# Optimization experiments

Hardware: AMD Instinct MI355X
Metric: run time of the kernel (lower is better)

Reference implementation:

```python
import jax, jax.numpy as jnp
import numpy as np

N_LAYERS = 4
D = 768
H = 12
DK = D // H
FF = 2048
SD = 5
DIM_LOC = 6
EPS = 1e-10


def layer_norm(x, g, b, eps=1e-5):
    m = x.mean(-1, keepdims=True)
    v = ((x - m) ** 2).mean(-1, keepdims=True)
    return (x - m) / jnp.sqrt(v + eps) * g + b


def calc_pairwise_locs(centers):
    # centers: [b, l, 3] -> [b, l, t, 5] spatial relation features ('center' type, dist-normalized)
    rel = centers[:, :, None, :] - centers[:, None, :, :]
    d = jnp.sqrt(jnp.sum(rel ** 2, -1) + EPS)
    max_d = jnp.max(d.reshape(d.shape[0], -1), -1)
    dn = d / max_d[:, None, None]
    d2 = jnp.sqrt(jnp.sum(rel[..., :2] ** 2, -1) + EPS)
    return jnp.stack([dn, rel[..., 2] / d, d2 / d, rel[..., 1] / d2, rel[..., 0] / d2], -1)


def setup_inputs() -> dict:
    key = jax.random.key(0)
    ks = jax.random.split(key, 32)
    B, L = 16, 512
    std = 0.02
    inp = {
        'obj_embeds': jax.random.normal(ks[0], (B, L, D), jnp.float32),
        'obj_locs': jax.random.uniform(ks[1], (B, L, DIM_LOC), jnp.float32) * 5.0,
        'obj_masks': jnp.ones((B, L), jnp.bool_),
        # single loc layer (obj_loc_encoding='same_all')
        'loc_w': jax.random.normal(ks[2], (DIM_LOC, D), jnp.float32) * std,
        'loc_b': jnp.zeros((D,), jnp.float32),
        'loc_ln_g': jnp.ones((D,), jnp.float32),
        'loc_ln_b': jnp.zeros((D,), jnp.float32),
        # per-layer params, stacked on leading layer dim
        'Wq': jax.random.normal(ks[3], (N_LAYERS, D, D), jnp.float32) * std,
        'bq': jnp.zeros((N_LAYERS, D), jnp.float32),
        'Wk': jax.random.normal(ks[4], (N_LAYERS, D, D), jnp.float32) * std,
        'bk': jnp.zeros((N_LAYERS, D), jnp.float32),
        'Wv': jax.random.normal(ks[5], (N_LAYERS, D, D), jnp.float32) * std,
        'bv': jnp.zeros((N_LAYERS, D), jnp.float32),
        'Wfc': jax.random.normal(ks[6], (N_LAYERS, D, D), jnp.float32) * std,
        'bfc': jnp.zeros((N_LAYERS, D), jnp.float32),
        'loc_fc_w': jax.random.normal(ks[7], (N_LAYERS, SD, H), jnp.float32) * std,
        'loc_fc_b': jnp.zeros((N_LAYERS, H), jnp.float32),
        'ln0_g': jnp.ones((N_LAYERS, D), jnp.float32),
        'ln0_b': jnp.zeros((N_LAYERS, D), jnp.float32),
        'W1': jax.random.normal(ks[8], (N_LAYERS, D, FF), jnp.float32) * std,
        'b1': jnp.zeros((N_LAYERS, FF), jnp.float32),
        'W2': jax.random.normal(ks[9], (N_LAYERS, FF, D), jnp.float32) * std,
        'b2': jnp.zeros((N_LAYERS, D), jnp.float32),
        'ln1_g': jnp.ones((N_LAYERS, D), jnp.float32),
        'ln1_b': jnp.zeros((N_LAYERS, D), jnp.float32),
        'ln2_g': jnp.ones((N_LAYERS, D), jnp.float32),
        'ln2_b': jnp.zeros((N_LAYERS, D), jnp.float32),
    }
    return inp


def _forward(obj_embeds, obj_locs, obj_masks, loc_w, loc_b, loc_ln_g, loc_ln_b,
             Wq, bq, Wk, bk, Wv, bv, Wfc, bfc, loc_fc_w, loc_fc_b, ln0_g, ln0_b,
             W1, b1, W2, b2, ln1_g, ln1_b, ln2_g, ln2_b):
    B, L, _ = obj_embeds.shape
    pl = calc_pairwise_locs(obj_locs[..., :3])        # [b,l,t,5]
    kpm = jnp.logical_not(obj_masks)                  # key_padding_mask: True = pad
    mask = kpm[:, None, None, :]                      # [b,1,1,t]
    query_pos = layer_norm(obj_locs @ loc_w + loc_b, loc_ln_g, loc_ln_b)
    x = obj_embeds
    scale = np.float32(1.0 / np.sqrt(DK))
    for i in range(N_LAYERS):
        x = x + query_pos  # obj_loc_encoding='same_all': add loc embedding every layer
        res = x
        q = (x @ Wq[i] + bq[i]).reshape(B, L, H, DK)
        k = (x @ Wk[i] + bk[i]).reshape(B, L, H, DK)
        v = (x @ Wv[i] + bv[i]).reshape(B, L, H, DK)
        attn = jnp.einsum('blhk,bthk->bhlt', q, k) * scale
        loc_attn = jax.nn.relu(jnp.einsum('bltd,dh->bhlt', pl, loc_fc_w[i])
                               + loc_fc_b[i][None, :, None, None])
        attn = jnp.where(mask, -1e30, attn)
        loc_attn = jnp.where(mask, 0.0, loc_attn)
        fused = jax.nn.softmax(jnp.log(jnp.clip(loc_attn, 1e-6)) + attn, axis=-1)
        out = jnp.einsum('bhlt,bthv->blhv', fused, v).reshape(B, L, D)
        out = out @ Wfc[i] + bfc[i]
        x2 = layer_norm(out + res, ln0_g[i], ln0_b[i])   # attn-internal residual + LN
        x = layer_norm(x + x2, ln1_g[i], ln1_b[i])       # encoder-layer norm1
        ff = jax.nn.gelu(x @ W1[i] + b1[i], approximate=False) @ W2[i] + b2[i]
        x = layer_norm(x + ff, ln2_g[i], ln2_b[i])       # encoder-layer norm2
    return x


def reference(obj_embeds, obj_locs, obj_masks, loc_w, loc_b, loc_ln_g, loc_ln_b,
              Wq, bq, Wk, bk, Wv, bv, Wfc, bfc, loc_fc_w, loc_fc_b, ln0_g, ln0_b,
              W1, b1, W2, b2, ln1_g, ln1_b, ln2_g, ln2_b):
    return _forward(obj_embeds, obj_locs, obj_masks, loc_w, loc_b, loc_ln_g, loc_ln_b,
                    Wq, bq, Wk, bk, Wv, bv, Wfc, bfc, loc_fc_w, loc_fc_b, ln0_g, ln0_b,
                    W1, b1, W2, b2, ln1_g, ln1_b, ln2_g, ln2_b)
```

## Files before the change

### kernel.cpp

```cpp
#include <hip/hip_runtime.h>
#include <hip/hip_bf16.h>
#include <math.h>

#define NL 4
#define D 768
#define H 12
#define DK 64
#define FF 2048
#define SD 5
#define DLOC 6
#define B 16
#define L 512
#define M (B*L)

typedef unsigned short u16;
typedef unsigned int u32;
typedef __attribute__((ext_vector_type(8))) __bf16 bf16x8;
typedef __attribute__((ext_vector_type(4))) float f32x4;

__device__ inline float b2f(u16 u){ u32 v = ((u32)u)<<16; return __builtin_bit_cast(float, v); }
__device__ inline u16 f2b(float f){ __hip_bfloat16 h = __float2bfloat16(f); return __builtin_bit_cast(u16, h); }

__device__ inline void gld16(const u16* g, u16* l) {
    __builtin_amdgcn_global_load_lds(
        (const __attribute__((address_space(1))) u32*)(const void*)g,
        (__attribute__((address_space(3))) u32*)(void*)l, 16, 0, 0);
}

__global__ __launch_bounds__(256) void maxd_kernel(const float* __restrict__ locs,
                                                   u32* __restrict__ maxd) {
    int b = blockIdx.x >> 5;
    int seg = blockIdx.x & 31;
    __shared__ float cx[L], cy[L], cz[L];
    for (int i = threadIdx.x; i < L; i += 256) {
        const float* p = locs + ((size_t)b*L + i)*DLOC;
        cx[i] = p[0]; cy[i] = p[1]; cz[i] = p[2];
    }
    __syncthreads();
    float mx = 0.f;
    int r0 = seg*16;
    #pragma unroll
    for (int r = 0; r < 16; ++r) {
        float px = cx[r0+r], py = cy[r0+r], pz = cz[r0+r];
        for (int c = threadIdx.x; c < L; c += 256) {
            float dx = px-cx[c], dy = py-cy[c], dz = pz-cz[c];
            mx = fmaxf(mx, dx*dx + dy*dy + dz*dz);
        }
    }
    #pragma unroll
    for (int m=1;m<64;m<<=1) mx = fmaxf(mx, __shfl_xor(mx, m));
    __shared__ float wred[4];
    if ((threadIdx.x & 63) == 0) wred[threadIdx.x >> 6] = mx;
    __syncthreads();
    if (threadIdx.x == 0) {
        float v = fmaxf(fmaxf(wred[0],wred[1]), fmaxf(wred[2],wred[3]));
        float d = sqrtf(v + 1e-10f);
        atomicMax(maxd + b, __builtin_bit_cast(u32, d));
    }
}

__global__ __launch_bounds__(256) void initq_kernel(const float* __restrict__ embeds,
    const float* __restrict__ locs, const float* __restrict__ lw, const float* __restrict__ lb,
    const float* __restrict__ lg, const float* __restrict__ lbb,
    float* __restrict__ x, u16* __restrict__ xb) {
    int row = blockIdx.x;
    float lc[DLOC];
    #pragma unroll
    for (int d=0; d<DLOC; d++) lc[d] = locs[(size_t)row*DLOC + d];
    float mv[3], s1 = 0.f, s2 = 0.f;
    #pragma unroll
    for (int e = 0; e < 3; e++) {
        int col = threadIdx.x + 256*e;
        float v = lb[col];
        #pragma unroll
        for (int d = 0; d < DLOC; d++) v += lc[d]*lw[d*D + col];
        mv[e] = v; s1 += v; s2 += v*v;
    }
    __shared__ float r1[256], r2[256];
    r1[threadIdx.x]=s1; r2[threadIdx.x]=s2; __syncthreads();
    for (int s=128;s>0;s>>=1){
        if(threadIdx.x<s){r1[threadIdx.x]+=r1[threadIdx.x+s]; r2[threadIdx.x]+=r2[threadIdx.x+s];}
        __syncthreads();
    }
    float mean = r1[0]*(1.0f/D);
    float var  = r2[0]*(1.0f/D) - mean*mean;
    float rstd = rsqrtf(var + 1e-5f);
    #pragma unroll
    for (int e=0;e<3;e++){
        int col = threadIdx.x+256*e;
        float qp = (mv[e]-mean)*rstd*lg[col]+lbb[col];
        float v = embeds[(size_t)row*D+col] + qp;
        x[(size_t)row*D+col] = v;
        xb[(size_t)row*D+col] = f2b(v);
    }
}

__global__ __launch_bounds__(256) void ln01_kernel(const float* __restrict__ t0f,
    const float* __restrict__ xin,
    const float* __restrict__ g0, const float* __restrict__ b0,
    const float* __restrict__ g1, const float* __restrict__ b1,
    float* __restrict__ xout, u16* __restrict__ xb) {
    int row = blockIdx.x;
    __shared__ float r1[256], r2[256];
    float xv[3], vv[3], s1=0.f, s2=0.f;
    #pragma unroll
    for (int e=0;e<3;e++){
        int col = threadIdx.x+256*e;
        float xr = xin[(size_t)row*D+col];
        float v = t0f[(size_t)row*D+col] + xr;
        xv[e]=xr; vv[e]=v; s1+=v; s2+=v*v;
    }
    r1[threadIdx.x]=s1; r2[threadIdx.x]=s2; __syncthreads();
    for (int s=128;s>0;s>>=1){
        if(threadIdx.x<s){r1[threadIdx.x]+=r1[threadIdx.x+s]; r2[threadIdx.x]+=r2[threadIdx.x+s];}
        __syncthreads();
    }
    float mean0 = r1[0]*(1.0f/D);
    float var0  = r2[0]*(1.0f/D) - mean0*mean0;
    float rstd0 = rsqrtf(var0 + 1e-5f);
    __syncthreads();
    float uv[3]; s1=0.f; s2=0.f;
    #pragma unroll
    for (int e=0;e<3;e++){
        int col = threadIdx.x+256*e;
        float x2 = (vv[e]-mean0)*rstd0*g0[col]+b0[col];
        float u = xv[e] + x2;
        uv[e]=u; s1+=u; s2+=u*u;
    }
    r1[threadIdx.x]=s1; r2[threadIdx.x]=s2; __syncthreads();
    for (int s=128;s>0;s>>=1){
        if(threadIdx.x<s){r1[threadIdx.x]+=r1[threadIdx.x+s]; r2[threadIdx.x]+=r2[threadIdx.x+s];}
        __syncthreads();
    }
    float mean1 = r1[0]*(1.0f/D);
    float var1  = r2[0]*(1.0f/D) - mean1*mean1;
    float rstd1 = rsqrtf(var1 + 1e-5f);
    #pragma unroll
    for (int e=0;e<3;e++){
        int col = threadIdx.x+256*e;
        float v = (uv[e]-mean1)*rstd1*g1[col]+b1[col];
        xout[(size_t)row*D+col] = v;
        xb[(size_t)row*D+col] = f2b(v);
    }
}

template<int LAST>
__global__ __launch_bounds__(256) void ln2q_kernel(const float* __restrict__ xin,
    const float* __restrict__ t0f, const float* __restrict__ g2, const float* __restrict__ b2,
    const float* __restrict__ locs, const float* __restrict__ lw, const float* __restrict__ lb,
    const float* __restrict__ lg, const float* __restrict__ lbb,
    float* __restrict__ xout, u16* __restrict__ xb) {
    int row = blockIdx.x;
    __shared__ float r1[256], r2[256], r3[256], r4[256];
    float lc[DLOC];
    if (!LAST) {
        #pragma unroll
        for (int d=0; d<DLOC; d++) lc[d] = locs[(size_t)row*DLOC + d];
    }
    float vv[3], mv[3], s1=0.f, s2=0.f, s3=0.f, s4=0.f;
    #pragma unroll
    for (int e=0;e<3;e++){
        int col = threadIdx.x+256*e;
        float v = xin[(size_t)row*D+col] + t0f[(size_t)row*D+col];
        vv[e]=v; s1+=v; s2+=v*v;
        if (!LAST) {
            float mvv = lb[col];
            #pragma unroll
            for (int d = 0; d < DLOC; d++) mvv += lc[d]*lw[d*D + col];
            mv[e]=mvv; s3+=mvv; s4+=mvv*mvv;
        }
    }
    r1[threadIdx.x]=s1; r2[threadIdx.x]=s2;
    if (!LAST) { r3[threadIdx.x]=s3; r4[threadIdx.x]=s4; }
    __syncthreads();
    for (int s=128;s>0;s>>=1){
        if(threadIdx.x<s){
            r1[threadIdx.x]+=r1[threadIdx.x+s]; r2[threadIdx.x]+=r2[threadIdx.x+s];
            if (!LAST){ r3[threadIdx.x]+=r3[threadIdx.x+s]; r4[threadIdx.x]+=r4[threadIdx.x+s]; }
        }
        __syncthreads();
    }
    float mean = r1[0]*(1.0f/D);
    float var  = r2[0]*(1.0f/D) - mean*mean;
    float rstd = rsqrtf(var + 1e-5f);
    float mean3=0.f, rstd3=0.f;
    if (!LAST) {
        mean3 = r3[0]*(1.0f/D);
        float var3 = r4[0]*(1.0f/D) - mean3*mean3;
        rstd3 = rsqrtf(var3 + 1e-5f);
    }
    #pragma unroll
    for (int e=0;e<3;e++){
        int col = threadIdx.x+256*e;
        float xn = (vv[e]-mean)*rstd*g2[col]+b2[col];
        if (LAST) {
            xout[(size_t)row*D+col] = xn;
        } else {
            float qp = (mv[e]-mean3)*rstd3*lg[col]+lbb[col];
            float v = xn + qp;
            xout[(size_t)row*D+col] = v;
            xb[(size_t)row*D+col] = f2b(v);
        }
    }
}

__global__ __launch_bounds__(256) void convT6_kernel(
    const float* __restrict__ Wq, const float* __restrict__ Wk,
    const float* __restrict__ Wv, const float* __restrict__ Wfc,
    const float* __restrict__ W1, const float* __restrict__ W2,
    u16* __restrict__ wq_t, u16* __restrict__ wfc_t,
    u16* __restrict__ w1_t, u16* __restrict__ w2_t) {
    int bid = blockIdx.x;
    const float* in; u16* outp; int K, N, nb, kb;
    if (bid < 1728) {
        int m = bid / 576, r = bid % 576;
        in = (m==0) ? Wq : (m==1) ? Wk : Wv;
        outp = wq_t + m*D*D; K = D; N = D; nb = r % 24; kb = r / 24;
    } else if (bid < 2304) {
        int r = bid - 1728;
        in = Wfc; outp = wfc_t; K = D; N = D; nb = r % 24; kb = r / 24;
    } else if (bid < 3840) {
        int r = bid - 2304;
        in = W1; outp = w1_t; K = D; N = FF; nb = r % 64; kb = r / 64;
    } else {
        int r = bid - 3840;
        in = W2; outp = w2_t; K = FF; N = D; nb = r % 24; kb = r / 24;
    }
    __shared__ float tile[32][33];
    int kbb = kb*32, nbb = nb*32;
    int tx = threadIdx.x & 31, ty = threadIdx.x >> 5;
    #pragma unroll
    for (int i=0;i<32;i+=8)
        tile[ty+i][tx] = in[(size_t)(kbb+ty+i)*N + nbb+tx];
    __syncthreads();
    #pragma unroll
    for (int i=0;i<32;i+=8)
        outp[(size_t)(nbb+ty+i)*K + kbb+tx] = f2b(tile[tx][ty+i]);
}

__global__ __launch_bounds__(256) void biaspack_kernel(const float* __restrict__ bq,
    const float* __restrict__ bk, const float* __restrict__ bv, float* __restrict__ outb) {
    int i = blockIdx.x*256 + threadIdx.x;
    int l = i / (3*D), j = i % (3*D);
    float v = (j < D) ? bq[l*D + j] : (j < 2*D ? bk[l*D + j - D] : bv[l*D + j - 2*D]);
    outb[i] = v;
}

template<int OUT_BF16, int ACT>
__global__ __launch_bounds__(256) void mm_kernel(
    const u16* __restrict__ A, const u16* __restrict__ Bt,
    const float* __restrict__ bias, void* __restrict__ Cout, int K, int N)
{
    __shared__ u16 As[2][128*32];
    __shared__ u16 Bs[2][128*32];
    const int tid = threadIdx.x;
    const int lane = tid & 63, wv = tid >> 6;
    const int m0 = blockIdx.y*128, n0 = blockIdx.x*128;
    const int wm = (wv>>1)*64, wn = (wv&1)*64;

    const u16* ag = A  + (size_t)(m0 + wv*16 + (lane>>2))*K + (lane&3)*8;
    const u16* bg = Bt + (size_t)(n0 + wv*16 + (lane>>2))*K + (lane&3)*8;
    const size_t rstep = (size_t)64*K;
    const int lofs = wv*512;

    f32x4 acc[4][4];
    #pragma unroll
    for (int i=0;i<4;i++)
        #pragma unroll
        for (int j=0;j<4;j++) acc[i][j] = (f32x4){0.f,0.f,0.f,0.f};

    const int lr = lane & 15, kq = lane >> 4;

    gld16(ag, &As[0][lofs]);
    gld16(ag + rstep, &As[0][2048+lofs]);
    gld16(bg, &Bs[0][lofs]);
    gld16(bg + rstep, &Bs[0][2048+lofs]);
    __syncthreads();

    int cur = 0;
    for (int k0 = 0; k0 < K; k0 += 32) {
        if (k0 + 32 < K) {
            int nx = cur ^ 1, kn = k0 + 32;
            gld16(ag + kn, &As[nx][lofs]);
            gld16(ag + rstep + kn, &As[nx][2048+lofs]);
            gld16(bg + kn, &Bs[nx][lofs]);
            gld16(bg + rstep + kn, &Bs[nx][2048+lofs]);
        }
        const u16* Arow = &As[cur][(wm + lr)*32 + kq*8];
        const u16* Brow = &Bs[cur][(wn + lr)*32 + kq*8];
        bf16x8 af[4], bfr[4];
        #pragma unroll
        for (int i=0;i<4;i++) af[i]  = *(const bf16x8*)(Arow + i*512);
        #pragma unroll
        for (int j=0;j<4;j++) bfr[j] = *(const bf16x8*)(Brow + j*512);
        #pragma unroll
        for (int i=0;i<4;i++)
            #pragma unroll
            for (int j=0;j<4;j++)
                acc[i][j] = __builtin_amdgcn_mfma_f32_16x16x32_bf16(af[i], bfr[j], acc[i][j], 0,0,0);
        __syncthreads();
        cur ^= 1;
    }

    const int cr = (lane>>4)*4, cc = lane & 15;
    #pragma unroll
    for (int i=0;i<4;i++) {
        int row = m0 + wm + i*16 + cr;
        #pragma unroll
        for (int j=0;j<4;j++) {
            int col = n0 + wn + j*16 + cc;
            float bv_ = bias[col];
            #pragma unroll
            for (int r=0;r<4;r++) {
                float v = acc[i][j][r] + bv_;
                if (ACT) v = 0.5f*v*(1.0f + erff(v*0.70710678f));
                if (OUT_BF16) ((u16*)Cout)[(size_t)(row+r)*N + col] = f2b(v);
                else        ((float*)Cout)[(size_t)(row+r)*N + col] = v;
            }
        }
    }
}

__global__ __launch_bounds__(256) void attn_kernel(
    const u16* __restrict__ qkv, const float* __restrict__ locs,
    const float* __restrict__ maxdp, const float* __restrict__ lfw,
    const float* __restrict__ lfb, u16* __restrict__ out)
{
    const int RS = 3*D;
    const float SC = 0.18033688f;
    const int bid = blockIdx.x;
    const int qt = bid & 7;
    const int hp = (bid >> 3) % 6;
    const int b  = bid / 48;
    const int qb = qt*64;
    const int h0 = hp*2;

    __shared__ u16 Ks[2][64*64];
    __shared__ u16 Vt[2][64*64];
    __shared__ u16 Pl[2][4*16*64];
    __shared__ float Cts[64][4];

    const int t = threadIdx.x;
    const int lane = t & 63, wv = t >> 6;
    const int l15 = lane & 15, l4 = lane >> 4;

    bf16x8 qf[2][2];
    {
        const u16* qr = qkv + (size_t)(b*L + qb + wv*16 + l15)*RS + h0*DK + l4*8;
        qf[0][0] = *(const bf16x8*)(qr);
        qf[0][1] = *(const bf16x8*)(qr + 32);
        qf[1][0] = *(const bf16x8*)(qr + DK);
        qf[1][1] = *(const bf16x8*)(qr + DK + 32);
    }
    float cqx[4], cqy[4], cqz[4];
    #pragma unroll
    for (int r=0;r<4;r++){
        const float* p = locs + (size_t)(b*L + qb + wv*16 + l4*4 + r)*DLOC;
        cqx[r]=p[0]; cqy[r]=p[1]; cqz[r]=p[2];
    }
    const float invmd = 1.0f / maxdp[b];
    float w0p[2], w1[2], w2[2], w3[2], w4[2], wbb[2];
    #pragma unroll
    for (int hh=0; hh<2; hh++){
        int h = h0+hh;
        w0p[hh] = lfw[0*H+h]*invmd; w1[hh]=lfw[1*H+h]; w2[hh]=lfw[2*H+h];
        w3[hh]=lfw[3*H+h]; w4[hh]=lfw[4*H+h]; wbb[hh]=lfb[h];
    }

    f32x4 oacc[2][4];
    float mrun[2][4], lrun[2][4];
    #pragma unroll
    for (int hh=0;hh<2;hh++)
        #pragma unroll
        for (int j=0;j<4;j++){ oacc[hh][j] = (f32x4){0.f,0.f,0.f,0.f};
                               mrun[hh][j] = -1e30f; lrun[hh][j] = 0.f; }

    const int srow0 = (wv*64 + lane) >> 3;
    const int sslot = lane & 7;

    for (int kt = 0; kt < L; kt += 64) {
        const u16* kgb = qkv + (size_t)(b*L + kt)*RS + D + h0*DK;
        {
            int r0 = srow0, r1 = srow0 + 32;
            int c0 = (sslot ^ (r0&7))*8, c1 = (sslot ^ (r1&7))*8;
            gld16(kgb + (size_t)r0*RS + c0, &Ks[0][wv*512]);
            gld16(kgb + (size_t)r1*RS + c1, &Ks[0][2048 + wv*512]);
            gld16(kgb + DK + (size_t)r0*RS + c0, &Ks[1][wv*512]);
            gld16(kgb + DK + (size_t)r1*RS + c1, &Ks[1][2048 + wv*512]);
        }
        #pragma unroll
        for (int hh=0; hh<2; hh++){
            const u16* vp = qkv + (size_t)(b*L + kt + lane)*RS + 2*D + (h0+hh)*DK + wv*16;
            bf16x8 v0 = *(const bf16x8*)(vp);
            bf16x8 v1 = *(const bf16x8*)(vp + 8);
            int d0 = wv*16;
            #pragma unroll
            for (int e=0;e<8;e++){
                Vt[hh][(d0+e)*64   + (lane ^ (e<<3))] = ((const u16*)&v0)[e];
                Vt[hh][(d0+8+e)*64 + (lane ^ (e<<3))] = ((const u16*)&v1)[e];
            }
        }
        if (t < 64) {
            #pragma unroll
            for (int d=0;d<3;d++) Cts[t][d] = locs[(size_t)(b*L + kt + t)*DLOC + d];
        }
        __syncthreads();

        f32x4 sacc[2][4];
        #pragma unroll
        for (int hh=0;hh<2;hh++)
            #pragma unroll
            for (int j=0;j<4;j++){
                sacc[hh][j] = (f32x4){0.f,0.f,0.f,0.f};
                #pragma unroll
                for (int c=0;c<2;c++){
                    int row = j*16 + l15;
                    int slot = l4 + 4*c;
                    bf16x8 kf = *(const bf16x8*)(&Ks[hh][row*64 + ((slot ^ (row&7))*8)]);
                    sacc[hh][j] = __builtin_amdgcn_mfma_f32_16x16x32_bf16(qf[hh][c], kf, sacc[hh][j], 0,0,0);
                }
            }

        float ctx[4], cty[4], ctz[4];
        #pragma unroll
        for (int j=0;j<4;j++){
            int c = l15 + 16*j;
            ctx[j]=Cts[c][0]; cty[j]=Cts[c][1]; ctz[j]=Cts[c][2];
        }

        float alr[2][4];
        #pragma unroll
        for (int r=0;r<4;r++){
            float f0[4], f1[4], f2[4], f3[4], f4[4];
            #pragma unroll
            for (int j=0;j<4;j++){
                float rx = cqx[r]-ctx[j], ry = cqy[r]-cty[j], rz = cqz[r]-ctz[j];
                float d2e = fmaf(ry,ry, fmaf(rx,rx, 1e-10f));
                float r2  = fmaf(rz,rz, d2e);
                float invd  = __builtin_amdgcn_rsqf(r2);
                float invd2 = __builtin_amdgcn_rsqf(d2e);
                f0[j] = r2*invd;
                f1[j] = rz*invd;
                f2[j] = (d2e*invd2)*invd;
                f3[j] = ry*invd2;
                f4[j] = rx*invd2;
            }
            #pragma unroll
            for (int hh=0; hh<2; hh++){
                float sv[4], la[4];
                #pragma unroll
                for (int j=0;j<4;j++){
                    float z = fmaf(f0[j], w0p[hh],
                              fmaf(f1[j], w1[hh],
                              fmaf(f2[j], w2[hh],
                              fmaf(f3[j], w3[hh],
                              fmaf(f4[j], w4[hh], wbb[hh])))));
                    la[j] = fmaxf(z, 1e-6f);
                    sv[j] = sacc[hh][j][r]*SC;
                }
                float mx = fmaxf(fmaxf(sv[0],sv[1]), fmaxf(sv[2],sv[3]));
                #pragma unroll
                for (int msk=1; msk<16; msk<<=1) mx = fmaxf(mx, __shfl_xor(mx, msk));
                float mo = mrun[hh][r];
                float mn = fmaxf(mo, mx);
                float al = __builtin_amdgcn_exp2f(mo - mn);
                float sp = 0.f;
                u16* pw = &Pl[hh][wv*1024];
                int q = l4*4 + r, sw = (q&7)<<3;
                #pragma unroll
                for (int j=0;j<4;j++){
                    float p = la[j] * __builtin_amdgcn_exp2f(sv[j] - mn);
                    sp += p;
                    pw[q*64 + ((l15 + 16*j) ^ sw)] = f2b(p);
                }
                #pragma unroll
                for (int msk=1; msk<16; msk<<=1) sp += __shfl_xor(sp, msk);
                mrun[hh][r] = mn;
                lrun[hh][r] = lrun[hh][r]*al + sp;
                alr[hh][r] = al;
            }
        }

        #pragma unroll
        for (int hh=0; hh<2; hh++){
            #pragma unroll
            for (int j=0;j<4;j++)
                #pragma unroll
                for (int r=0;r<4;r++) oacc[hh][j][r] *= alr[hh][r];
            const u16* pr = &Pl[hh][wv*1024];
            #pragma unroll
            for (int c=0;c<2;c++){
                int prow = l15;
                int pslot = l4 + 4*c;
                bf16x8 pf = *(const bf16x8*)(pr + prow*64 + ((pslot ^ (prow&7))*8));
                #pragma unroll
                for (int j=0;j<4;j++){
                    int vrow = j*16 + l15;
                    int vslot = l4 + 4*c;
                    bf16x8 vf = *(const bf16x8*)(&Vt[hh][vrow*64 + ((vslot ^ (vrow&7))*8)]);
                    oacc[hh][j] = __builtin_amdgcn_mfma_f32_16x16x32_bf16(pf, vf, oacc[hh][j], 0,0,0);
                }
            }
        }
        __syncthreads();
    }

    #pragma unroll
    for (int hh=0; hh<2; hh++)
        #pragma unroll
        for (int r=0;r<4;r++){
            float inv = __builtin_amdgcn_rcpf(lrun[hh][r]);
            size_t obase = (size_t)(b*L + qb + wv*16 + l4*4 + r)*D + (h0+hh)*DK;
            #pragma unroll
            for (int j=0;j<4;j++)
                out[obase + l15 + 16*j] = f2b(oacc[hh][j][r] * inv);
        }
}

extern "C" void kernel_launch(void* const* d_in, const int* in_sizes, int n_in,
                              void* d_out, int out_size, void* d_ws, size_t ws_size,
                              hipStream_t stream) {
    const float* obj_embeds = (const float*)d_in[0];
    const float* obj_locs   = (const float*)d_in[1];
    const float* loc_w   = (const float*)d_in[3];
    const float* loc_b   = (const float*)d_in[4];
    const float* loc_ln_g= (const float*)d_in[5];
    const float* loc_ln_b= (const float*)d_in[6];
    const float* Wq = (const float*)d_in[7];
    const float* bq = (const float*)d_in[8];
    const float* Wk = (const float*)d_in[9];
    const float* bk = (const float*)d_in[10];
    const float* Wv = (const float*)d_in[11];
    const float* bv = (const float*)d_in[12];
    const float* Wfc= (const float*)d_in[13];
    const float* bfc= (const float*)d_in[14];
    const float* lfw= (const float*)d_in[15];
    const float* lfb= (const float*)d_in[16];
    const float* ln0_g = (const float*)d_in[17];
    const float* ln0_b = (const float*)d_in[18];
    const float* W1 = (const float*)d_in[19];
    const float* b1 = (const float*)d_in[20];
    const float* W2 = (const float*)d_in[21];
    const float* b2 = (const float*)d_in[22];
    const float* ln1_g = (const float*)d_in[23];
    const float* ln1_b = (const float*)d_in[24];
    const float* ln2_g = (const float*)d_in[25];
    const float* ln2_b = (const float*)d_in[26];

    float* x  = (float*)d_out;
    char* base = (char*)d_ws;
    u16*   xb    = (u16*)  (base);
    u16*   qkv   = (u16*)  (base + 12582912);
    u16*   aob   = (u16*)  (base + 50331648);
    float* t0f   = (float*)(base + 62914560);
    u16*   wq_t  = (u16*)  (base + 88080384);
    u16*   wfc_t = (u16*)  (base + 91619328);
    u16*   w1_t  = (u16*)  (base + 92798976);
    u16*   w2_t  = (u16*)  (base + 95944704);
    float* bqkv  = (float*)(base + 99090432);
    u32*   maxd  = (u32*)  (base + 99127296);
    u16*   h1b   = qkv;

    hipMemsetAsync(maxd, 0, B*sizeof(u32), stream);
    maxd_kernel<<<B*32, 256, 0, stream>>>(obj_locs, maxd);
    biaspack_kernel<<<(NL*3*D)/256, 256, 0, stream>>>(bq, bk, bv, bqkv);
    initq_kernel<<<M, 256, 0, stream>>>(obj_embeds, obj_locs, loc_w, loc_b,
                                        loc_ln_g, loc_ln_b, x, xb);

    for (int i = 0; i < NL; i++) {
        const size_t wo = (size_t)i*D*D;
        convT6_kernel<<<5376, 256, 0, stream>>>(Wq + wo, Wk + wo, Wv + wo, Wfc + wo,
                                                W1 + (size_t)i*D*FF, W2 + (size_t)i*FF*D,
                                                wq_t, wfc_t, w1_t, w2_t);

        mm_kernel<1,0><<<dim3(18,64), 256, 0, stream>>>(xb, wq_t, bqkv + i*3*D, qkv, D, 3*D);
        attn_kernel<<<B*6*8, 256, 0, stream>>>(qkv, obj_locs, (const float*)maxd,
                                               lfw + i*SD*H, lfb + i*H, aob);
        mm_kernel<0,0><<<dim3(6,64), 256, 0, stream>>>(aob, wfc_t, bfc + i*D, t0f, D, D);
        ln01_kernel<<<M, 256, 0, stream>>>(t0f, x, ln0_g + i*D, ln0_b + i*D,
                                           ln1_g + i*D, ln1_b + i*D, x, xb);
        mm_kernel<1,1><<<dim3(16,64), 256, 0, stream>>>(xb, w1_t, b1 + i*FF, h1b, D, FF);
        mm_kernel<0,0><<<dim3(6,64), 256, 0, stream>>>(h1b, w2_t, b2 + i*D, t0f, FF, D);
        if (i < NL-1)
            ln2q_kernel<0><<<M, 256, 0, stream>>>(x, t0f, ln2_g + i*D, ln2_b + i*D,
                obj_locs, loc_w, loc_b, loc_ln_g, loc_ln_b, x, xb);
        else
            ln2q_kernel<1><<<M, 256, 0, stream>>>(x, t0f, ln2_g + i*D, ln2_b + i*D,
                obj_locs, loc_w, loc_b, loc_ln_g, loc_ln_b, x, xb);
    }
}
```

Baseline: 1.214 ms.

## Vectorize layernorm kernels, widen weight transpose, remap GEMM tile order

The layernorm-style kernels (initq, ln01, ln2q) now use 192 threads, each handling four contiguous columns through float4 loads and stores. Their block reductions use wavefront shuffles and one small shared-memory step instead of a tree of __syncthreads. The weight transpose kernel uses float4 reads and ushort4 bf16 writes. The GEMM kernel remaps block IDs so consecutive blocks are spread across eight groups, likely to fit the MI355X's multiple-XCD layout and improve L2 locality. The aim is fewer memory transactions and less sync overhead in bandwidth-bound elementwise kernels, at the cost of extra remapping arithmetic and the assumption that grid sizes divide by 8.

```diff
diff --git a/kernel.cpp b/kernel.cpp
--- a/kernel.cpp
+++ b/kernel.cpp
@@ -59,148 +59,161 @@
     }
 }
 
-__global__ __launch_bounds__(256) void initq_kernel(const float* __restrict__ embeds,
+__global__ __launch_bounds__(192) void initq_kernel(const float* __restrict__ embeds,
     const float* __restrict__ locs, const float* __restrict__ lw, const float* __restrict__ lb,
     const float* __restrict__ lg, const float* __restrict__ lbb,
     float* __restrict__ x, u16* __restrict__ xb) {
     int row = blockIdx.x;
+    int c4 = threadIdx.x*4;
+    int lane = threadIdx.x & 63, wv = threadIdx.x >> 6;
     float lc[DLOC];
     #pragma unroll
     for (int d=0; d<DLOC; d++) lc[d] = locs[(size_t)row*DLOC + d];
-    float mv[3], s1 = 0.f, s2 = 0.f;
-    #pragma unroll
-    for (int e = 0; e < 3; e++) {
-        int col = threadIdx.x + 256*e;
-        float v = lb[col];
-        #pragma unroll
-        for (int d = 0; d < DLOC; d++) v += lc[d]*lw[d*D + col];
-        mv[e] = v; s1 += v; s2 += v*v;
-    }
-    __shared__ float r1[256], r2[256];
-    r1[threadIdx.x]=s1; r2[threadIdx.x]=s2; __syncthreads();
-    for (int s=128;s>0;s>>=1){
-        if(threadIdx.x<s){r1[threadIdx.x]+=r1[threadIdx.x+s]; r2[threadIdx.x]+=r2[threadIdx.x+s];}
-        __syncthreads();
-    }
-    float mean = r1[0]*(1.0f/D);
-    float var  = r2[0]*(1.0f/D) - mean*mean;
-    float rstd = rsqrtf(var + 1e-5f);
-    #pragma unroll
-    for (int e=0;e<3;e++){
-        int col = threadIdx.x+256*e;
-        float qp = (mv[e]-mean)*rstd*lg[col]+lbb[col];
-        float v = embeds[(size_t)row*D+col] + qp;
-        x[(size_t)row*D+col] = v;
-        xb[(size_t)row*D+col] = f2b(v);
-    }
-}
-
-__global__ __launch_bounds__(256) void ln01_kernel(const float* __restrict__ t0f,
+    float4 mv = *(const float4*)(lb + c4);
+    #pragma unroll
+    for (int d=0; d<DLOC; d++) {
+        float4 w = *(const float4*)(lw + d*D + c4);
+        mv.x = fmaf(lc[d], w.x, mv.x); mv.y = fmaf(lc[d], w.y, mv.y);
+        mv.z = fmaf(lc[d], w.z, mv.z); mv.w = fmaf(lc[d], w.w, mv.w);
+    }
+    float s1 = mv.x+mv.y+mv.z+mv.w;
+    float s2 = mv.x*mv.x+mv.y*mv.y+mv.z*mv.z+mv.w*mv.w;
+    #pragma unroll
+    for (int m=1;m<64;m<<=1){ s1 += __shfl_xor(s1,m); s2 += __shfl_xor(s2,m); }
+    __shared__ float a1[3], a2[3];
+    if (lane==0){ a1[wv]=s1; a2[wv]=s2; }
+    __syncthreads();
+    float S1 = a1[0]+a1[1]+a1[2], S2 = a2[0]+a2[1]+a2[2];
+    float mean = S1*(1.0f/D);
+    float rstd = rsqrtf(S2*(1.0f/D) - mean*mean + 1e-5f);
+    float4 G = *(const float4*)(lg + c4);
+    float4 Bb = *(const float4*)(lbb + c4);
+    float4 E = *(const float4*)(embeds + (size_t)row*D + c4);
+    float4 v;
+    v.x = E.x + (mv.x-mean)*rstd*G.x+Bb.x;
+    v.y = E.y + (mv.y-mean)*rstd*G.y+Bb.y;
+    v.z = E.z + (mv.z-mean)*rstd*G.z+Bb.z;
+    v.w = E.w + (mv.w-mean)*rstd*G.w+Bb.w;
+    *(float4*)(x + (size_t)row*D + c4) = v;
+    ushort4 u; u.x=f2b(v.x); u.y=f2b(v.y); u.z=f2b(v.z); u.w=f2b(v.w);
+    *(ushort4*)(xb + (size_t)row*D + c4) = u;
+}
+
+__global__ __launch_bounds__(192) void ln01_kernel(const float* __restrict__ t0f,
     const float* __restrict__ xin,
     const float* __restrict__ g0, const float* __restrict__ b0,
     const float* __restrict__ g1, const float* __restrict__ b1,
     float* __restrict__ xout, u16* __restrict__ xb) {
     int row = blockIdx.x;
-    __shared__ float r1[256], r2[256];
-    float xv[3], vv[3], s1=0.f, s2=0.f;
-    #pragma unroll
-    for (int e=0;e<3;e++){
-        int col = threadIdx.x+256*e;
-        float xr = xin[(size_t)row*D+col];
-        float v = t0f[(size_t)row*D+col] + xr;
-        xv[e]=xr; vv[e]=v; s1+=v; s2+=v*v;
-    }
-    r1[threadIdx.x]=s1; r2[threadIdx.x]=s2; __syncthreads();
-    for (int s=128;s>0;s>>=1){
-        if(threadIdx.x<s){r1[threadIdx.x]+=r1[threadIdx.x+s]; r2[threadIdx.x]+=r2[threadIdx.x+s];}
-        __syncthreads();
-    }
-    float mean0 = r1[0]*(1.0f/D);
-    float var0  = r2[0]*(1.0f/D) - mean0*mean0;
-    float rstd0 = rsqrtf(var0 + 1e-5f);
-    __syncthreads();
-    float uv[3]; s1=0.f; s2=0.f;
-    #pragma unroll
-    for (int e=0;e<3;e++){
-        int col = threadIdx.x+256*e;
-        float x2 = (vv[e]-mean0)*rstd0*g0[col]+b0[col];
-        float u = xv[e] + x2;
-        uv[e]=u; s1+=u; s2+=u*u;
-    }
-    r1[threadIdx.x]=s1; r2[threadIdx.x]=s2; __syncthreads();
-    for (int s=128;s>0;s>>=1){
-        if(threadIdx.x<s){r1[threadIdx.x]+=r1[threadIdx.x+s]; r2[threadIdx.x]+=r2[threadIdx.x+s];}
-        __syncthreads();
-    }
-    float mean1 = r1[0]*(1.0f/D);
-    float var1  = r2[0]*(1.0f/D) - mean1*mean1;
-    float rstd1 = rsqrtf(var1 + 1e-5f);
-    #pragma unroll
-    for (int e=0;e<3;e++){
-        int col = threadIdx.x+256*e;
-        float v = (uv[e]-mean1)*rstd1*g1[col]+b1[col];
-        xout[(size_t)row*D+col] = v;
-        xb[(size_t)row*D+col] = f2b(v);
-    }
+    int c4 = threadIdx.x*4;
+    int lane = threadIdx.x & 63, wv = threadIdx.x >> 6;
+    size_t base = (size_t)row*D + c4;
+    float4 xr = *(const float4*)(xin + base);
+    float4 tv = *(const float4*)(t0f + base);
+    float4 v = {xr.x+tv.x, xr.y+tv.y, xr.z+tv.z, xr.w+tv.w};
+    float s1 = v.x+v.y+v.z+v.w;
+    float s2 = v.x*v.x+v.y*v.y+v.z*v.z+v.w*v.w;
+    #pragma unroll
+    for (int m=1;m<64;m<<=1){ s1 += __shfl_xor(s1,m); s2 += __shfl_xor(s2,m); }
+    __shared__ float a1[3], a2[3], a3[3], a4[3];
+    if (lane==0){ a1[wv]=s1; a2[wv]=s2; }
+    __syncthreads();
+    float S1 = a1[0]+a1[1]+a1[2], S2 = a2[0]+a2[1]+a2[2];
+    float mean0 = S1*(1.0f/D);
+    float rstd0 = rsqrtf(S2*(1.0f/D) - mean0*mean0 + 1e-5f);
+    float4 G0 = *(const float4*)(g0 + c4);
+    float4 B0 = *(const float4*)(b0 + c4);
+    float4 u;
+    u.x = xr.x + (v.x-mean0)*rstd0*G0.x+B0.x;
+    u.y = xr.y + (v.y-mean0)*rstd0*G0.y+B0.y;
+    u.z = xr.z + (v.z-mean0)*rstd0*G0.z+B0.z;
+    u.w = xr.w + (v.w-mean0)*rstd0*G0.w+B0.w;
+    s1 = u.x+u.y+u.z+u.w;
+    s2 = u.x*u.x+u.y*u.y+u.z*u.z+u.w*u.w;
+    #pragma unroll
+    for (int m=1;m<64;m<<=1){ s1 += __shfl_xor(s1,m); s2 += __shfl_xor(s2,m); }
+    if (lane==0){ a3[wv]=s1; a4[wv]=s2; }
+    __syncthreads();
+    S1 = a3[0]+a3[1]+a3[2]; S2 = a4[0]+a4[1]+a4[2];
+    float mean1 = S1*(1.0f/D);
+    float rstd1 = rsqrtf(S2*(1.0f/D) - mean1*mean1 + 1e-5f);
+    float4 G1 = *(const float4*)(g1 + c4);
+    float4 B1 = *(const float4*)(b1 + c4);
+    float4 o;
+    o.x = (u.x-mean1)*rstd1*G1.x+B1.x;
+    o.y = (u.y-mean1)*rstd1*G1.y+B1.y;
+    o.z = (u.z-mean1)*rstd1*G1.z+B1.z;
+    o.w = (u.w-mean1)*rstd1*G1.w+B1.w;
+    *(float4*)(xout + base) = o;
+    ushort4 ub; ub.x=f2b(o.x); ub.y=f2b(o.y); ub.z=f2b(o.z); ub.w=f2b(o.w);
+    *(ushort4*)(xb + base) = ub;
 }
 
 template<int LAST>
-__global__ __launch_bounds__(256) void ln2q_kernel(const float* __restrict__ xin,
+__global__ __launch_bounds__(192) void ln2q_kernel(const float* __restrict__ xin,
     const float* __restrict__ t0f, const float* __restrict__ g2, const float* __restrict__ b2,
     const float* __restrict__ locs, const float* __restrict__ lw, const float* __restrict__ lb,
     const float* __restrict__ lg, const float* __restrict__ lbb,
     float* __restrict__ xout, u16* __restrict__ xb) {
     int row = blockIdx.x;
-    __shared__ float r1[256], r2[256], r3[256], r4[256];
-    float lc[DLOC];
+    int c4 = threadIdx.x*4;
+    int lane = threadIdx.x & 63, wv = threadIdx.x >> 6;
+    size_t base = (size_t)row*D + c4;
+    float4 xr = *(const float4*)(xin + base);
+    float4 tv = *(const float4*)(t0f + base);
+    float4 v = {xr.x+tv.x, xr.y+tv.y, xr.z+tv.z, xr.w+tv.w};
+    float s1 = v.x+v.y+v.z+v.w;
+    float s2 = v.x*v.x+v.y*v.y+v.z*v.z+v.w*v.w;
+    float s3 = 0.f, s4 = 0.f;
+    float4 mv = {0,0,0,0};
     if (!LAST) {
+        float lc[DLOC];
         #pragma unroll
         for (int d=0; d<DLOC; d++) lc[d] = locs[(size_t)row*DLOC + d];
-    }
-    float vv[3], mv[3], s1=0.f, s2=0.f, s3=0.f, s4=0.f;
-    #pragma unroll
-    for (int e=0;e<3;e++){
-        int col = threadIdx.x+256*e;
-        float v = xin[(size_t)row*D+col] + t0f[(size_t)row*D+col];
-        vv[e]=v; s1+=v; s2+=v*v;
-        if (!LAST) {
-            float mvv = lb[col];
-            #pragma unroll
-            for (int d = 0; d < DLOC; d++) mvv += lc[d]*lw[d*D + col];
-            mv[e]=mvv; s3+=mvv; s4+=mvv*mvv;
-        }
-    }
-    r1[threadIdx.x]=s1; r2[threadIdx.x]=s2;
-    if (!LAST) { r3[threadIdx.x]=s3; r4[threadIdx.x]=s4; }
-    __syncthreads();
-    for (int s=128;s>0;s>>=1){
-        if(threadIdx.x<s){
-            r1[threadIdx.x]+=r1[threadIdx.x+s]; r2[threadIdx.x]+=r2[threadIdx.x+s];
-            if (!LAST){ r3[threadIdx.x]+=r3[threadIdx.x+s]; r4[threadIdx.x]+=r4[threadIdx.x+s]; }
-        }
-        __syncthreads();
-    }
-    float mean = r1[0]*(1.0f/D);
-    float var  = r2[0]*(1.0f/D) - mean*mean;
-    float rstd = rsqrtf(var + 1e-5f);
-    float mean3=0.f, rstd3=0.f;
-    if (!LAST) {
-        mean3 = r3[0]*(1.0f/D);
-        float var3 = r4[0]*(1.0f/D) - mean3*mean3;
-        rstd3 = rsqrtf(var3 + 1e-5f);
-    }
-    #pragma unroll
-    for (int e=0;e<3;e++){
-        int col = threadIdx.x+256*e;
-        float xn = (vv[e]-mean)*rstd*g2[col]+b2[col];
-        if (LAST) {
-            xout[(size_t)row*D+col] = xn;
-        } else {
-            float qp = (mv[e]-mean3)*rstd3*lg[col]+lbb[col];
-            float v = xn + qp;
-            xout[(size_t)row*D+col] = v;
-            xb[(size_t)row*D+col] = f2b(v);
-        }
+        mv = *(const float4*)(lb + c4);
+        #pragma unroll
+        for (int d=0; d<DLOC; d++) {
+            float4 w = *(const float4*)(lw + d*D + c4);
+            mv.x = fmaf(lc[d], w.x, mv.x); mv.y = fmaf(lc[d], w.y, mv.y);
+            mv.z = fmaf(lc[d], w.z, mv.z); mv.w = fmaf(lc[d], w.w, mv.w);
+        }
+        s3 = mv.x+mv.y+mv.z+mv.w;
+        s4 = mv.x*mv.x+mv.y*mv.y+mv.z*mv.z+mv.w*mv.w;
+    }
+    #pragma unroll
+    for (int m=1;m<64;m<<=1){
+        s1 += __shfl_xor(s1,m); s2 += __shfl_xor(s2,m);
+        if (!LAST){ s3 += __shfl_xor(s3,m); s4 += __shfl_xor(s4,m); }
+    }
+    __shared__ float a1[3], a2[3], a3[3], a4[3];
+    if (lane==0){ a1[wv]=s1; a2[wv]=s2; if(!LAST){ a3[wv]=s3; a4[wv]=s4; } }
+    __syncthreads();
+    float S1 = a1[0]+a1[1]+a1[2], S2 = a2[0]+a2[1]+a2[2];
+    float mean = S1*(1.0f/D);
+    float rstd = rsqrtf(S2*(1.0f/D) - mean*mean + 1e-5f);
+    float4 G2 = *(const float4*)(g2 + c4);
+    float4 B2 = *(const float4*)(b2 + c4);
+    float4 xn;
+    xn.x = (v.x-mean)*rstd*G2.x+B2.x;
+    xn.y = (v.y-mean)*rstd*G2.y+B2.y;
+    xn.z = (v.z-mean)*rstd*G2.z+B2.z;
+    xn.w = (v.w-mean)*rstd*G2.w+B2.w;
+    if (LAST) {
+        *(float4*)(xout + base) = xn;
+    } else {
+        float S3 = a3[0]+a3[1]+a3[2], S4 = a4[0]+a4[1]+a4[2];
+        float mean3 = S3*(1.0f/D);
+        float rstd3 = rsqrtf(S4*(1.0f/D) - mean3*mean3 + 1e-5f);
+        float4 G = *(const float4*)(lg + c4);
+        float4 Bb = *(const float4*)(lbb + c4);
+        float4 o;
+        o.x = xn.x + (mv.x-mean3)*rstd3*G.x+Bb.x;
+        o.y = xn.y + (mv.y-mean3)*rstd3*G.y+Bb.y;
+        o.z = xn.z + (mv.z-mean3)*rstd3*G.z+Bb.z;
+        o.w = xn.w + (mv.w-mean3)*rstd3*G.w+Bb.w;
+        *(float4*)(xout + base) = o;
+        ushort4 ub; ub.x=f2b(o.x); ub.y=f2b(o.y); ub.z=f2b(o.z); ub.w=f2b(o.w);
+        *(ushort4*)(xb + base) = ub;
     }
 }
 
@@ -228,14 +241,21 @@
     }
     __shared__ float tile[32][33];
     int kbb = kb*32, nbb = nb*32;
-    int tx = threadIdx.x & 31, ty = threadIdx.x >> 5;
-    #pragma unroll
-    for (int i=0;i<32;i+=8)
-        tile[ty+i][tx] = in[(size_t)(kbb+ty+i)*N + nbb+tx];
-    __syncthreads();
-    #pragma unroll
-    for (int i=0;i<32;i+=8)
-        outp[(size_t)(nbb+ty+i)*K + kbb+tx] = f2b(tile[tx][ty+i]);
+    int tq = threadIdx.x & 7, tr = threadIdx.x >> 3;
+    {
+        float4 vv = *(const float4*)(in + (size_t)(kbb+tr)*N + nbb + tq*4);
+        tile[tr][tq*4+0] = vv.x; tile[tr][tq*4+1] = vv.y;
+        tile[tr][tq*4+2] = vv.z; tile[tr][tq*4+3] = vv.w;
+    }
+    __syncthreads();
+    {
+        ushort4 ub;
+        ub.x = f2b(tile[tq*4+0][tr]);
+        ub.y = f2b(tile[tq*4+1][tr]);
+        ub.z = f2b(tile[tq*4+2][tr]);
+        ub.w = f2b(tile[tq*4+3][tr]);
+        *(ushort4*)(outp + (size_t)(nbb+tr)*K + kbb + tq*4) = ub;
+    }
 }
 
 __global__ __launch_bounds__(256) void biaspack_kernel(const float* __restrict__ bq,
@@ -255,7 +275,13 @@
     __shared__ u16 Bs[2][128*32];
     const int tid = threadIdx.x;
     const int lane = tid & 63, wv = tid >> 6;
-    const int m0 = blockIdx.y*128, n0 = blockIdx.x*128;
+
+    const int gx = gridDim.x;
+    const int id = blockIdx.y*gx + blockIdx.x;
+    const int q8 = (gx*gridDim.y) >> 3;
+    const int nid = (id & 7)*q8 + (id >> 3);
+    const int m0 = (nid / gx)*128, n0 = (nid % gx)*128;
+
     const int wm = (wv>>1)*64, wn = (wv&1)*64;
 
     const u16* ag = A  + (size_t)(m0 + wv*16 + (lane>>2))*K + (lane&3)*8;
@@ -564,7 +590,7 @@
     hipMemsetAsync(maxd, 0, B*sizeof(u32), stream);
     maxd_kernel<<<B*32, 256, 0, stream>>>(obj_locs, maxd);
     biaspack_kernel<<<(NL*3*D)/256, 256, 0, stream>>>(bq, bk, bv, bqkv);
-    initq_kernel<<<M, 256, 0, stream>>>(obj_embeds, obj_locs, loc_w, loc_b,
+    initq_kernel<<<M, 192, 0, stream>>>(obj_embeds, obj_locs, loc_w, loc_b,
                                         loc_ln_g, loc_ln_b, x, xb);
 
     for (int i = 0; i < NL; i++) {
@@ -577,15 +603,15 @@
         attn_kernel<<<B*6*8, 256, 0, stream>>>(qkv, obj_locs, (const float*)maxd,
                                                lfw + i*SD*H, lfb + i*H, aob);
         mm_kernel<0,0><<<dim3(6,64), 256, 0, stream>>>(aob, wfc_t, bfc + i*D, t0f, D, D);
-        ln01_kernel<<<M, 256, 0, stream>>>(t0f, x, ln0_g + i*D, ln0_b + i*D,
+        ln01_kernel<<<M, 192, 0, stream>>>(t0f, x, ln0_g + i*D, ln0_b + i*D,
                                            ln1_g + i*D, ln1_b + i*D, x, xb);
         mm_kernel<1,1><<<dim3(16,64), 256, 0, stream>>>(xb, w1_t, b1 + i*FF, h1b, D, FF);
         mm_kernel<0,0><<<dim3(6,64), 256, 0, stream>>>(h1b, w2_t, b2 + i*D, t0f, FF, D);
         if (i < NL-1)
-            ln2q_kernel<0><<<M, 256, 0, stream>>>(x, t0f, ln2_g + i*D, ln2_b + i*D,
+            ln2q_kernel<0><<<M, 192, 0, stream>>>(x, t0f, ln2_g + i*D, ln2_b + i*D,
                 obj_locs, loc_w, loc_b, loc_ln_g, loc_ln_b, x, xb);
         else
-            ln2q_kernel<1><<<M, 256, 0, stream>>>(x, t0f, ln2_g + i*D, ln2_b + i*D,
+            ln2q_kernel<1><<<M, 192, 0, stream>>>(x, t0f, ln2_g + i*D, ln2_b + i*D,
                 obj_locs, loc_w, loc_b, loc_ln_g, loc_ln_b, x, xb);
     }
 }
```

After: 1.155 ms. -4.9%, faster.
